# Optimization experiments

Hardware: AMD Instinct MI355X
Metric: run time of the kernel (lower is better)

Reference implementation:

```python
import jax, jax.numpy as jnp
import numpy as np

N, D = 8192, 1024


def setup_inputs() -> dict:
    key = jax.random.key(0)
    k1, k2 = jax.random.split(key)
    x = jax.random.normal(k1, (N, D), dtype=jnp.float32)
    # scale weight like a trained linear layer (~1/sqrt(D)) so softmax isn't fully saturated
    W = jax.random.normal(k2, (D, D), dtype=jnp.float32) * (1.0 / np.sqrt(D))
    b = jnp.zeros((D,), dtype=jnp.float32)
    recency_weight = jnp.full((1,), -0.5, dtype=jnp.float32)  # nn.Parameter init in source
    return {"x": x, "W": W, "b": b, "recency_weight": recency_weight}


def reference(x, W, b, recency_weight):
    # linear + relu
    x_proj = jax.nn.relu(x @ W.T + b)          # [N, D]
    # tied self-matmul
    scores = x_proj @ x_proj.T                  # [N, N]
    n = x.shape[0]
    idx = jnp.arange(n)
    # causal mask: upper triangle strictly above diagonal (use_current_timestep=True)
    upper = idx[None, :] > idx[:, None]         # [N, N] bool
    scores = jnp.where(upper, -jnp.inf, scores)
    # recency bias: toeplitz |i - j|, zeroed on masked (upper) part, scaled by recency_weight
    dist = jnp.abs(idx[:, None] - idx[None, :]).astype(scores.dtype)
    recency = recency_weight[0] * jnp.where(upper, 0.0, dist)
    scores = scores + recency
    return jax.nn.softmax(scores, axis=1)       # [N, N] lower-triangular attention
```

## Files before the change

kernel.cpp:

```cpp
#include <hip/hip_runtime.h>
#include <math.h>

#define NR 8192
#define DIM 1024

typedef __attribute__((ext_vector_type(8))) short bf16x8;
typedef __attribute__((ext_vector_type(4))) float f32x4;

static __device__ __forceinline__ unsigned short f2bf(float f) {
  unsigned int u = __float_as_uint(f);
  u += 0x7fffu + ((u >> 16) & 1u);
  return (unsigned short)(u >> 16);
}

static __device__ __forceinline__ void gload_lds16(const void* g, void* lds) {
  __builtin_amdgcn_global_load_lds(
      (const __attribute__((address_space(1))) unsigned int*)g,
      (__attribute__((address_space(3))) unsigned int*)lds, 16, 0, 0);
}

__global__ __launch_bounds__(256) void cvt_bf16(const float* __restrict__ in,
                                                unsigned short* __restrict__ outp,
                                                int n4) {
  int i = blockIdx.x * 256 + threadIdx.x;
  if (i < n4) {
    float4 v = ((const float4*)in)[i];
    ushort4 o;
    o.x = f2bf(v.x); o.y = f2bf(v.y); o.z = f2bf(v.z); o.w = f2bf(v.w);
    ((ushort4*)outp)[i] = o;
  }
}

static __device__ __forceinline__ void gemm_core(const unsigned short* A,
                                                 const unsigned short* B,
                                                 int m0, int n0, int K,
                                                 short* As, short* Bs,
                                                 f32x4 acc[4][4]) {
  const int tid  = threadIdx.x;
  const int lane = tid & 63;
  const int wave = tid >> 6;
  const int wr = wave >> 1, wc = wave & 1;
  const int ch_r = lane >> 2;
  const int ch_c = (lane & 3) * 8;

  for (int kt = 0; kt < K; kt += 32) {
#pragma unroll
    for (int c = 0; c < 4; ++c) {
      int ch = wave * 4 + c;
      if (ch < 8) {
        const unsigned short* g = A + (size_t)(m0 + ch * 16 + ch_r) * DIM + kt + ch_c;
        gload_lds16(g, As + ch * 512);
      } else {
        const unsigned short* g = B + (size_t)(n0 + (ch - 8) * 16 + ch_r) * DIM + kt + ch_c;
        gload_lds16(g, Bs + (ch - 8) * 512);
      }
    }
    asm volatile("s_waitcnt vmcnt(0)" ::: "memory");
    __syncthreads();

    bf16x8 af[4], bfr[4];
#pragma unroll
    for (int m = 0; m < 4; ++m)
      af[m] = *(const bf16x8*)(As + (wr * 64 + m * 16 + (lane & 15)) * 32 + (lane >> 4) * 8);
#pragma unroll
    for (int n = 0; n < 4; ++n)
      bfr[n] = *(const bf16x8*)(Bs + (wc * 64 + n * 16 + (lane & 15)) * 32 + (lane >> 4) * 8);
#pragma unroll
    for (int m = 0; m < 4; ++m)
#pragma unroll
      for (int n = 0; n < 4; ++n)
        acc[m][n] = __builtin_amdgcn_mfma_f32_16x16x32_bf16(af[m], bfr[n], acc[m][n], 0, 0, 0);
    __syncthreads();
  }
}

__global__ __launch_bounds__(256) void gemm1_relu(const unsigned short* __restrict__ Xb,
                                                  const unsigned short* __restrict__ Wb,
                                                  const float* __restrict__ bias,
                                                  unsigned short* __restrict__ XP) {
  __shared__ short As[4096], Bs[4096];
  const int m0 = blockIdx.y * 128, n0 = blockIdx.x * 128;
  f32x4 acc[4][4] = {};
  gemm_core(Xb, Wb, m0, n0, DIM, As, Bs, acc);

  const int lane = threadIdx.x & 63, wave = threadIdx.x >> 6;
  const int wr = wave >> 1, wc = wave & 1, g = lane >> 4, li = lane & 15;
#pragma unroll
  for (int m = 0; m < 4; ++m)
#pragma unroll
    for (int n = 0; n < 4; ++n) {
      int col = n0 + wc * 64 + n * 16 + li;
      float bv = bias[col];
#pragma unroll
      for (int r = 0; r < 4; ++r) {
        int row = m0 + wr * 64 + m * 16 + g * 4 + r;
        float v = fmaxf(acc[m][n][r] + bv, 0.0f);
        XP[(size_t)row * DIM + col] = f2bf(v);
      }
    }
}

__global__ __launch_bounds__(256) void gemm2_scores(const unsigned short* __restrict__ XP,
                                                    const float* __restrict__ rwp,
                                                    float* __restrict__ out,
                                                    float* __restrict__ wsm,
                                                    float* __restrict__ wsl) {
  const int bx = blockIdx.x, by = blockIdx.y;
  if (bx > by) return;
  __shared__ short As[4096], Bs[4096];
  const int m0 = by * 128, n0 = bx * 128;
  f32x4 acc[4][4] = {};
  gemm_core(XP, XP, m0, n0, DIM, As, Bs, acc);

  const float rw = rwp[0];
  const int lane = threadIdx.x & 63, wave = threadIdx.x >> 6;
  const int wr = wave >> 1, wc = wave & 1, g = lane >> 4, li = lane & 15;
  const int pcol = bx * 2 + wc;

#pragma unroll
  for (int m = 0; m < 4; ++m) {
#pragma unroll
    for (int r = 0; r < 4; ++r) {
      const int row = m0 + wr * 64 + m * 16 + g * 4 + r;
      float s[4];
      float mx = -INFINITY;
#pragma unroll
      for (int n = 0; n < 4; ++n) {
        int col = n0 + wc * 64 + n * 16 + li;
        float v = acc[m][n][r];
        if (col <= row) {
          v += rw * (float)(row - col);
          out[(size_t)row * NR + col] = v;
        } else {
          v = -INFINITY;
        }
        s[n] = v;
        mx = fmaxf(mx, v);
      }
#pragma unroll
      for (int off = 1; off < 16; off <<= 1) mx = fmaxf(mx, __shfl_xor(mx, off));
      float se = 0.0f;
#pragma unroll
      for (int n = 0; n < 4; ++n) se += __expf(s[n] - mx);
#pragma unroll
      for (int off = 1; off < 16; off <<= 1) se += __shfl_xor(se, off);
      if (li == 0) {
        wsm[(size_t)row * 128 + pcol] = mx;
        wsl[(size_t)row * 128 + pcol] = se;
      }
    }
  }
}

__global__ __launch_bounds__(256) void rowstats(const float* __restrict__ wsm,
                                                const float* __restrict__ wsl,
                                                float* __restrict__ Ms,
                                                float* __restrict__ Ls) {
  const int row = blockIdx.x * 4 + (threadIdx.x >> 6);
  const int lane = threadIdx.x & 63;
  const int nch = (row >> 6) + 1;
  float m0v = (lane < nch) ? wsm[(size_t)row * 128 + lane] : -INFINITY;
  float m1v = (lane + 64 < nch) ? wsm[(size_t)row * 128 + lane + 64] : -INFINITY;
  float mx = fmaxf(m0v, m1v);
#pragma unroll
  for (int off = 1; off < 64; off <<= 1) mx = fmaxf(mx, __shfl_xor(mx, off));
  float l = 0.0f;
  if (lane < nch)      l += wsl[(size_t)row * 128 + lane]      * __expf(m0v - mx);
  if (lane + 64 < nch) l += wsl[(size_t)row * 128 + lane + 64] * __expf(m1v - mx);
#pragma unroll
  for (int off = 1; off < 64; off <<= 1) l += __shfl_xor(l, off);
  if (lane == 0) { Ms[row] = mx; Ls[row] = 1.0f / l; }
}

__global__ __launch_bounds__(256) void normk(float* __restrict__ out,
                                             const float* __restrict__ Ms,
                                             const float* __restrict__ Ls) {
  const size_t idx = (size_t)blockIdx.x * 256 + threadIdx.x;
  const int row = (int)(idx >> 11);
  const int j0 = (int)(idx & 2047) * 4;
  float4* p = (float4*)out + idx;
  const float M = Ms[row], sc = Ls[row];
  if (j0 + 3 <= row) {
    float4 v = *p;
    v.x = __expf(v.x - M) * sc;
    v.y = __expf(v.y - M) * sc;
    v.z = __expf(v.z - M) * sc;
    v.w = __expf(v.w - M) * sc;
    *p = v;
  } else if (j0 > row) {
    float4 z; z.x = 0.f; z.y = 0.f; z.z = 0.f; z.w = 0.f;
    *p = z;
  } else {
    float4 v = *p;
    float4 o;
    o.x = (j0 + 0 <= row) ? __expf(v.x - M) * sc : 0.f;
    o.y = (j0 + 1 <= row) ? __expf(v.y - M) * sc : 0.f;
    o.z = (j0 + 2 <= row) ? __expf(v.z - M) * sc : 0.f;
    o.w = (j0 + 3 <= row) ? __expf(v.w - M) * sc : 0.f;
    *p = o;
  }
}

extern "C" void kernel_launch(void* const* d_in, const int* in_sizes, int n_in,
                              void* d_out, int out_size, void* d_ws, size_t ws_size,
                              hipStream_t stream) {
  const float* x  = (const float*)d_in[0];
  const float* W  = (const float*)d_in[1];
  const float* b  = (const float*)d_in[2];
  const float* rw = (const float*)d_in[3];
  float* out = (float*)d_out;

  char* ws = (char*)d_ws;
  unsigned short* Xb = (unsigned short*)(ws);
  unsigned short* Wb = (unsigned short*)(ws + (size_t)(16 << 20));
  unsigned short* XP = (unsigned short*)(ws + (size_t)(18 << 20));
  float* wsm = (float*)(ws + (size_t)(34 << 20));
  float* wsl = (float*)(ws + (size_t)(38 << 20));
  float* Ms  = (float*)(ws + (size_t)(42 << 20));
  float* Ls  = (float*)(ws + (size_t)(42 << 20) + 32768);

  cvt_bf16<<<NR * DIM / 4 / 256, 256, 0, stream>>>(x, Xb, NR * DIM / 4);
  cvt_bf16<<<DIM * DIM / 4 / 256, 256, 0, stream>>>(W, Wb, DIM * DIM / 4);
  gemm1_relu<<<dim3(DIM / 128, NR / 128), 256, 0, stream>>>(Xb, Wb, b, XP);
  gemm2_scores<<<dim3(NR / 128, NR / 128), 256, 0, stream>>>(XP, rw, out, wsm, wsl);
  rowstats<<<NR / 4, 256, 0, stream>>>(wsm, wsl, Ms, Ls);
  normk<<<(NR / 4) * (NR / 256), 256, 0, stream>>>(out, Ms, Ls);
}
```

Baseline: 492.2 us.

## Store bf16 partial exponentials in scores GEMM and launch only lower-triangle tiles

The scores GEMM now writes exp(s - local max) as bf16 into a workspace buffer instead of writing raw fp32 scores into the output. The normalize pass then reads those bf16 values and rescales them with a per-chunk factor from the saved partial max, so it no longer recomputes the exponential. The GEMM grid is also a 1D launch over only the lower-triangle tiles, with an interleaved mapping, instead of a 2D grid that exits early on upper tiles. This halves the intermediate traffic and removes idle blocks, at the cost of bf16 rounding on the unnormalized probabilities.

```diff
diff --git a/kernel.cpp b/kernel.cpp
--- a/kernel.cpp
+++ b/kernel.cpp
@@ -11,6 +11,10 @@
   unsigned int u = __float_as_uint(f);
   u += 0x7fffu + ((u >> 16) & 1u);
   return (unsigned short)(u >> 16);
+}
+
+static __device__ __forceinline__ float bf2f(unsigned short u) {
+  return __uint_as_float(((unsigned int)u) << 16);
 }
 
 static __device__ __forceinline__ void gload_lds16(const void* g, void* lds) {
@@ -102,11 +106,15 @@
 
 __global__ __launch_bounds__(256) void gemm2_scores(const unsigned short* __restrict__ XP,
                                                     const float* __restrict__ rwp,
-                                                    float* __restrict__ out,
+                                                    unsigned short* __restrict__ Pb,
                                                     float* __restrict__ wsm,
                                                     float* __restrict__ wsl) {
-  const int bx = blockIdx.x, by = blockIdx.y;
-  if (bx > by) return;
+  int t = ((int)blockIdx.x & 7) * 260 + ((int)blockIdx.x >> 3);
+  int by = (int)((sqrtf(8.0f * (float)t + 1.0f) - 1.0f) * 0.5f);
+  while ((by + 1) * (by + 2) / 2 <= t) ++by;
+  while (by * (by + 1) / 2 > t) --by;
+  const int bx = t - by * (by + 1) / 2;
+
   __shared__ short As[4096], Bs[4096];
   const int m0 = by * 128, n0 = bx * 128;
   f32x4 acc[4][4] = {};
@@ -128,12 +136,7 @@
       for (int n = 0; n < 4; ++n) {
         int col = n0 + wc * 64 + n * 16 + li;
         float v = acc[m][n][r];
-        if (col <= row) {
-          v += rw * (float)(row - col);
-          out[(size_t)row * NR + col] = v;
-        } else {
-          v = -INFINITY;
-        }
+        v = (col <= row) ? v + rw * (float)(row - col) : -INFINITY;
         s[n] = v;
         mx = fmaxf(mx, v);
       }
@@ -141,7 +144,12 @@
       for (int off = 1; off < 16; off <<= 1) mx = fmaxf(mx, __shfl_xor(mx, off));
       float se = 0.0f;
 #pragma unroll
-      for (int n = 0; n < 4; ++n) se += __expf(s[n] - mx);
+      for (int n = 0; n < 4; ++n) {
+        float e = __expf(s[n] - mx);
+        se += e;
+        int col = n0 + wc * 64 + n * 16 + li;
+        if (col <= row) Pb[(size_t)row * NR + col] = f2bf(e);
+      }
 #pragma unroll
       for (int off = 1; off < 16; off <<= 1) se += __shfl_xor(se, off);
       if (li == 0) {
@@ -172,33 +180,34 @@
   if (lane == 0) { Ms[row] = mx; Ls[row] = 1.0f / l; }
 }
 
-__global__ __launch_bounds__(256) void normk(float* __restrict__ out,
+__global__ __launch_bounds__(256) void normk(const unsigned short* __restrict__ Pb,
+                                             float* __restrict__ out,
                                              const float* __restrict__ Ms,
-                                             const float* __restrict__ Ls) {
+                                             const float* __restrict__ Ls,
+                                             const float* __restrict__ wsm) {
   const size_t idx = (size_t)blockIdx.x * 256 + threadIdx.x;
   const int row = (int)(idx >> 11);
   const int j0 = (int)(idx & 2047) * 4;
   float4* p = (float4*)out + idx;
-  const float M = Ms[row], sc = Ls[row];
-  if (j0 + 3 <= row) {
-    float4 v = *p;
-    v.x = __expf(v.x - M) * sc;
-    v.y = __expf(v.y - M) * sc;
-    v.z = __expf(v.z - M) * sc;
-    v.w = __expf(v.w - M) * sc;
-    *p = v;
-  } else if (j0 > row) {
+  if (j0 > row) {
     float4 z; z.x = 0.f; z.y = 0.f; z.z = 0.f; z.w = 0.f;
     *p = z;
-  } else {
-    float4 v = *p;
-    float4 o;
-    o.x = (j0 + 0 <= row) ? __expf(v.x - M) * sc : 0.f;
-    o.y = (j0 + 1 <= row) ? __expf(v.y - M) * sc : 0.f;
-    o.z = (j0 + 2 <= row) ? __expf(v.z - M) * sc : 0.f;
-    o.w = (j0 + 3 <= row) ? __expf(v.w - M) * sc : 0.f;
-    *p = o;
-  }
+    return;
+  }
+  const float M = Ms[row];
+  const float sc = __expf(wsm[(size_t)row * 128 + (j0 >> 6)] - M) * Ls[row];
+  ushort4 q = *(const ushort4*)(Pb + (size_t)row * NR + j0);
+  float4 o;
+  o.x = bf2f(q.x) * sc;
+  o.y = bf2f(q.y) * sc;
+  o.z = bf2f(q.z) * sc;
+  o.w = bf2f(q.w) * sc;
+  if (j0 + 3 > row) {
+    if (j0 + 1 > row) o.y = 0.f;
+    if (j0 + 2 > row) o.z = 0.f;
+    o.w = 0.f;
+  }
+  *p = o;
 }
 
 extern "C" void kernel_launch(void* const* d_in, const int* in_sizes, int n_in,
@@ -218,11 +227,12 @@
   float* wsl = (float*)(ws + (size_t)(38 << 20));
   float* Ms  = (float*)(ws + (size_t)(42 << 20));
   float* Ls  = (float*)(ws + (size_t)(42 << 20) + 32768);
+  unsigned short* Pb = (unsigned short*)(ws + (size_t)(64 << 20));
 
   cvt_bf16<<<NR * DIM / 4 / 256, 256, 0, stream>>>(x, Xb, NR * DIM / 4);
   cvt_bf16<<<DIM * DIM / 4 / 256, 256, 0, stream>>>(W, Wb, DIM * DIM / 4);
   gemm1_relu<<<dim3(DIM / 128, NR / 128), 256, 0, stream>>>(Xb, Wb, b, XP);
-  gemm2_scores<<<dim3(NR / 128, NR / 128), 256, 0, stream>>>(XP, rw, out, wsm, wsl);
+  gemm2_scores<<<2080, 256, 0, stream>>>(XP, rw, Pb, wsm, wsl);
   rowstats<<<NR / 4, 256, 0, stream>>>(wsm, wsl, Ms, Ls);
-  normk<<<(NR / 4) * (NR / 256), 256, 0, stream>>>(out, Ms, Ls);
-}
+  normk<<<(NR / 4) * (NR / 256), 256, 0, stream>>>(Pb, out, Ms, Ls, wsm);
+}
```

New measurement: 453.3 us. 7.9% less time.
